# Performance work log

Hardware: AMD Instinct MI355X
Metric: run time of the kernel (lower is better)

## Reference

```python
import jax, jax.numpy as jnp
import numpy as np


def log_g(x):
    # log(relu(x) + 0.5) for x >= 0, else -softplus(-x)
    pos = jnp.log(jnp.maximum(x, 0.0) + 0.5)
    neg = -jax.nn.softplus(-x)
    return jnp.where(x >= 0, pos, neg)


def parallel_scan_log(log_coeffs, log_values):
    # h_t = a_t * h_{t-1} + b_t, computed stably in log space
    a_star = jnp.cumsum(log_coeffs, axis=1)
    log_h0_plus_b_star = jax.lax.cumlogsumexp(log_values - a_star, axis=1)
    log_h = a_star + log_h0_plus_b_star
    return jnp.exp(log_h)


def setup_inputs() -> dict:
    key = jax.random.key(0)
    k1, k2 = jax.random.split(key)
    B, S, D = 8, 4096, 1024
    x = jax.random.normal(k1, (B, S, D), dtype=jnp.float32)
    # torch nn.Linear(dim, 2*inner_dim, bias=False): weight [2*inner_dim, dim]
    W_hg = jax.random.normal(k2, (2 * D, D), dtype=jnp.float32) * (1.0 / np.sqrt(D))
    return {"x": x, "W_hg": W_hg}


def reference(x, W_hg):
    # hidden_gate projection: [B,S,D] @ [D, 2*inner] -> [B,S,2*inner]
    hg = jnp.einsum("bsd,ed->bse", x, W_hg)
    hidden, gate = jnp.split(hg, 2, axis=-1)
    log_coeffs = -jax.nn.softplus(gate)       # log(1 - z)
    log_z = -jax.nn.softplus(-gate)           # log(z)
    log_tilde_h = log_g(hidden)
    log_values = log_z + log_tilde_h
    out = parallel_scan_log(log_coeffs, log_values)
    # expansion_factor == 1.0 -> self.out is Identity; dropout_prob == 0 -> Identity
    return out
```

## Files before the change

### kernel.cpp

```cpp
#include <hip/hip_runtime.h>

#define B_   8
#define S_   4096
#define D_   1024
#define M_   (B_ * S_)
#define N_   (2 * D_)
#define K_   D_
#define CCH  128
#define LCH  32

#define BK   64
#define NT   (K_ / BK)

typedef __attribute__((ext_vector_type(8))) short bf16x8;
typedef __attribute__((ext_vector_type(4))) float f32x4;

__device__ __forceinline__ unsigned short f2bf(float f) {
  union { float f; unsigned u; } v; v.f = f;
  unsigned u = v.u;
  u = u + 0x7fffu + ((u >> 16) & 1u);
  return (unsigned short)(u >> 16);
}
__device__ __forceinline__ float bf2f(unsigned short h) {
  union { unsigned u; float f; } v; v.u = ((unsigned)h) << 16;
  return v.f;
}
__device__ __forceinline__ float sigmoidf_(float x) {
  return 1.0f / (1.0f + __expf(-x));
}

#define GLL(src, dst) __builtin_amdgcn_global_load_lds(                     \
      (const __attribute__((address_space(1))) void*)(src),                 \
      (__attribute__((address_space(3))) void*)(dst), 16, 0, 0)

__global__ __launch_bounds__(256) void k_cvt(const float* __restrict__ in,
                                             unsigned short* __restrict__ out,
                                             int n4) {
  int i = blockIdx.x * 256 + threadIdx.x;
  const int stride = gridDim.x * 256;
  for (; i < n4; i += stride) {
    float4 v = reinterpret_cast<const float4*>(in)[i];
    ushort4 o;
    o.x = f2bf(v.x); o.y = f2bf(v.y); o.z = f2bf(v.z); o.w = f2bf(v.w);
    reinterpret_cast<ushort4*>(out)[i] = o;
  }
}

__global__ __launch_bounds__(512, 2) void k_gemm(const unsigned short* __restrict__ xb,
                                                 const unsigned short* __restrict__ wb,
                                                 unsigned short* __restrict__ Gp,
                                                 unsigned short* __restrict__ Zp) {
  __shared__ unsigned short lds[65536];
  const int tid = threadIdx.x;
  int wg = blockIdx.x;
  wg = (wg & 7) * 128 + (wg >> 3);
  const int bm = wg >> 3;
  const int bn = wg & 7;
  const int lane = tid & 63;
  const int wid = tid >> 6;
  const int wr = wid >> 2;
  const int wc = wid & 3;
  const int fr = lane & 15;
  const int hi = lane >> 4;
  const int f7 = fr & 7;

  const int srow = tid >> 3;
  const int scol = ((tid & 7) ^ (srow & 7)) * 16;
  const char* aS = (const char*)xb + (size_t)(bm * 256 + srow) * 2048 + scol;
  const char* bS = (const char*)wb + (size_t)(bn * 256 + srow) * 2048 + scol;
  char* const ldsc = (char*)lds + (size_t)tid * 16;

  const int swz0 = (hi ^ f7) * 8;
  const int swz1 = ((4 + hi) ^ f7) * 8;

  f32x4 acc[8][4] = {};
  bf16x8 av[4], bv[4];

#define RD_BV(SWZ)                                                           \
  _Pragma("unroll") for (int n = 0; n < 4; ++n)                              \
    bv[n] = *(const bf16x8*)&Bb[(wc * 64 + n * 16 + fr) * 64 + (SWZ)];
#define RD_AV(MB, SWZ)                                                       \
  _Pragma("unroll") for (int m = 0; m < 4; ++m)                              \
    av[m] = *(const bf16x8*)&Ab[(wr * 128 + (MB) * 64 + m * 16 + fr) * 64 + (SWZ)];

#define STAGE4(srcbase, region)                                              \
  if (st) {                                                                  \
    GLL((srcbase) + kb,                  ldsc + bufN + (region));            \
    GLL((srcbase) + 131072 + kb,         ldsc + bufN + (region) + 8192);     \
    GLL((srcbase) + 262144 + kb,         ldsc + bufN + (region) + 16384);    \
    GLL((srcbase) + 393216 + kb,         ldsc + bufN + (region) + 24576);    \
  }

#define PHASE16(M0)                                                          \
  __builtin_amdgcn_s_barrier();                                              \
  asm volatile("s_waitcnt lgkmcnt(0)" ::: "memory");                         \
  __builtin_amdgcn_s_setprio(1);                                             \
  _Pragma("unroll") for (int m = 0; m < 4; ++m)                              \
    _Pragma("unroll") for (int n = 0; n < 4; ++n)                            \
      acc[(M0) + m][n] = __builtin_amdgcn_mfma_f32_16x16x32_bf16(            \
          av[m], bv[n], acc[(M0) + m][n], 0, 0, 0);                          \
  __builtin_amdgcn_s_setprio(0);

#pragma unroll
  for (int c = 0; c < 4; ++c) {
    GLL(aS + (size_t)c * 131072, ldsc + c * 8192);
    GLL(bS + (size_t)c * 131072, ldsc + 32768 + c * 8192);
  }
  asm volatile("s_waitcnt vmcnt(0)" ::: "memory");
  __builtin_amdgcn_s_barrier();

  for (int t = 0; t < NT; ++t) {
    const unsigned short* Ab = &lds[(t & 1) << 15];
    const unsigned short* Bb = Ab + 16384;
    const int bufN = ((t + 1) & 1) << 16;
    const size_t kb = (size_t)(t + 1) * 128;
    const bool st = (t < NT - 1);

    RD_BV(swz0);
    RD_AV(0, swz0);
    STAGE4(aS, 0);
    PHASE16(0);
    __builtin_amdgcn_s_barrier();

    RD_AV(1, swz0);
    STAGE4(bS, 32768);
    PHASE16(4);
    __builtin_amdgcn_s_barrier();

    RD_BV(swz1);
    RD_AV(0, swz1);
    PHASE16(0);
    __builtin_amdgcn_s_barrier();

    RD_AV(1, swz1);
    PHASE16(4);
    asm volatile("s_waitcnt vmcnt(0)" ::: "memory");
    __builtin_amdgcn_s_barrier();
  }

  const int row0 = bm * 256 + wr * 128 + (hi << 2);
  const int col0 = bn * 256 + wc * 64 + fr;
  if (bn < 4) {
#pragma unroll
    for (int m = 0; m < 8; ++m)
#pragma unroll
      for (int n = 0; n < 4; ++n)
#pragma unroll
        for (int i = 0; i < 4; ++i) {
          float v = acc[m][n][i];
          float g = (v >= 0.0f) ? (v + 0.5f) : sigmoidf_(v);
          Gp[(size_t)(row0 + m * 16 + i) * 1024 + (col0 + n * 16)] = f2bf(g);
        }
  } else {
#pragma unroll
    for (int m = 0; m < 8; ++m)
#pragma unroll
      for (int n = 0; n < 4; ++n)
#pragma unroll
        for (int i = 0; i < 4; ++i) {
          float v = acc[m][n][i];
          Zp[(size_t)(row0 + m * 16 + i) * 1024 + (col0 + n * 16 - 1024)] = f2bf(sigmoidf_(v));
        }
  }
}

__global__ __launch_bounds__(256) void k_scan1(const unsigned short* __restrict__ Gp,
                                               const unsigned short* __restrict__ Zp,
                                               float* __restrict__ Ap,
                                               float* __restrict__ Hp) {
  const int gid = blockIdx.x * 256 + threadIdx.x;
  const int c = blockIdx.y;
  const int b = gid >> 8;
  const int d0 = (gid & 255) << 2;
  size_t base = ((size_t)b * S_ + (size_t)c * LCH) * 1024 + d0;
  float4 aP = {1.f, 1.f, 1.f, 1.f};
  float4 h  = {0.f, 0.f, 0.f, 0.f};
#pragma unroll 8
  for (int s = 0; s < LCH; ++s) {
    ushort4 zu = *reinterpret_cast<const ushort4*>(Zp + base);
    ushort4 gu = *reinterpret_cast<const ushort4*>(Gp + base);
    float z0 = bf2f(zu.x), z1 = bf2f(zu.y), z2 = bf2f(zu.z), z3 = bf2f(zu.w);
    float a0 = 1.f - z0,   a1 = 1.f - z1,   a2 = 1.f - z2,   a3 = 1.f - z3;
    h.x = fmaf(a0, h.x, z0 * bf2f(gu.x));
    h.y = fmaf(a1, h.y, z1 * bf2f(gu.y));
    h.z = fmaf(a2, h.z, z2 * bf2f(gu.z));
    h.w = fmaf(a3, h.w, z3 * bf2f(gu.w));
    aP.x *= a0; aP.y *= a1; aP.z *= a2; aP.w *= a3;
    base += 1024;
  }
  reinterpret_cast<float4*>(Ap)[(size_t)c * 2048 + gid] = aP;
  reinterpret_cast<float4*>(Hp)[(size_t)c * 2048 + gid] = h;
}

__global__ __launch_bounds__(256) void k_scan2(const float* __restrict__ Ap,
                                               const float* __restrict__ Hp,
                                               float* __restrict__ Cin) {
  const int gid = blockIdx.x * 256 + threadIdx.x;
  float4 carry = {0.f, 0.f, 0.f, 0.f};
  for (int c = 0; c < CCH; ++c) {
    reinterpret_cast<float4*>(Cin)[(size_t)c * 2048 + gid] = carry;
    float4 a = reinterpret_cast<const float4*>(Ap)[(size_t)c * 2048 + gid];
    float4 hh = reinterpret_cast<const float4*>(Hp)[(size_t)c * 2048 + gid];
    carry.x = fmaf(a.x, carry.x, hh.x);
    carry.y = fmaf(a.y, carry.y, hh.y);
    carry.z = fmaf(a.z, carry.z, hh.z);
    carry.w = fmaf(a.w, carry.w, hh.w);
  }
}

__global__ __launch_bounds__(256) void k_scan3(const unsigned short* __restrict__ Gp,
                                               const unsigned short* __restrict__ Zp,
                                               const float* __restrict__ Cin,
                                               float* __restrict__ out) {
  const int gid = blockIdx.x * 256 + threadIdx.x;
  const int c = blockIdx.y;
  const int b = gid >> 8;
  const int d0 = (gid & 255) << 2;
  size_t base = ((size_t)b * S_ + (size_t)c * LCH) * 1024 + d0;
  float4 h = reinterpret_cast<const float4*>(Cin)[(size_t)c * 2048 + gid];
#pragma unroll 8
  for (int s = 0; s < LCH; ++s) {
    ushort4 zu = *reinterpret_cast<const ushort4*>(Zp + base);
    ushort4 gu = *reinterpret_cast<const ushort4*>(Gp + base);
    float z0 = bf2f(zu.x), z1 = bf2f(zu.y), z2 = bf2f(zu.z), z3 = bf2f(zu.w);
    h.x = fmaf(1.f - z0, h.x, z0 * bf2f(gu.x));
    h.y = fmaf(1.f - z1, h.y, z1 * bf2f(gu.y));
    h.z = fmaf(1.f - z2, h.z, z2 * bf2f(gu.z));
    h.w = fmaf(1.f - z3, h.w, z3 * bf2f(gu.w));
    *reinterpret_cast<float4*>(out + base) = h;
    base += 1024;
  }
}

extern "C" void kernel_launch(void* const* d_in, const int* in_sizes, int n_in,
                              void* d_out, int out_size, void* d_ws, size_t ws_size,
                              hipStream_t stream) {
  const float* x = (const float*)d_in[0];
  const float* W = (const float*)d_in[1];
  float* out = (float*)d_out;

  unsigned char* w = (unsigned char*)d_ws;
  unsigned short* xb = (unsigned short*)(w);
  unsigned short* wb = (unsigned short*)(w + 67108864);
  unsigned short* Gp = (unsigned short*)(w + 67108864 + 4194304);
  unsigned short* Zp = (unsigned short*)(w + 67108864 + 4194304 + 67108864);
  float* Ap  = (float*)(w);
  float* Hp  = (float*)(w + 4194304);
  float* Cin = (float*)(w + 8388608);

  k_cvt<<<4096, 256, 0, stream>>>(x, xb, (M_ * K_) / 4);
  k_cvt<<<2048, 256, 0, stream>>>(W, wb, (N_ * K_) / 4);
  k_gemm<<<(M_ / 256) * (N_ / 256), 512, 0, stream>>>(xb, wb, Gp, Zp);
  k_scan1<<<dim3(8, CCH), 256, 0, stream>>>(Gp, Zp, Ap, Hp);
  k_scan2<<<8, 256, 0, stream>>>(Ap, Hp, Cin);
  k_scan3<<<dim3(8, CCH), 256, 0, stream>>>(Gp, Zp, Cin, out);
}
```

Baseline: 273.9 us.

## Double-buffer LDS fragment registers to overlap reads with MFMA and cut barriers

Restructures the GEMM main loop so LDS-to-register fragment loads for the next MFMA phase are issued while the current phase computes. Two register sets per operand are used, and the first fragments of the next k-tile are prefetched before the last MFMA phase. This drops most of the per-phase barriers and lgkmcnt waits. The cost is higher VGPR pressure from the extra fragment registers, which may hurt occupancy or cause spills. It also relies on compiler-inserted waits for correctness.

```diff
diff --git a/kernel.cpp b/kernel.cpp
--- a/kernel.cpp
+++ b/kernel.cpp
@@ -69,36 +69,22 @@
   const char* aS = (const char*)xb + (size_t)(bm * 256 + srow) * 2048 + scol;
   const char* bS = (const char*)wb + (size_t)(bn * 256 + srow) * 2048 + scol;
   char* const ldsc = (char*)lds + (size_t)tid * 16;
-
-  const int swz0 = (hi ^ f7) * 8;
-  const int swz1 = ((4 + hi) ^ f7) * 8;
+  const char* const ldsr = (const char*)lds;
+
+  const int aoff = (wr * 128 + fr) * 128;
+  const int boff = (wc * 64 + fr) * 128;
+  const int s0 = (hi ^ f7) * 16;
+  const int s1 = ((4 + hi) ^ f7) * 16;
 
   f32x4 acc[8][4] = {};
-  bf16x8 av[4], bv[4];
-
-#define RD_BV(SWZ)                                                           \
-  _Pragma("unroll") for (int n = 0; n < 4; ++n)                              \
-    bv[n] = *(const bf16x8*)&Bb[(wc * 64 + n * 16 + fr) * 64 + (SWZ)];
-#define RD_AV(MB, SWZ)                                                       \
-  _Pragma("unroll") for (int m = 0; m < 4; ++m)                              \
-    av[m] = *(const bf16x8*)&Ab[(wr * 128 + (MB) * 64 + m * 16 + fr) * 64 + (SWZ)];
-
-#define STAGE4(srcbase, region)                                              \
-  if (st) {                                                                  \
-    GLL((srcbase) + kb,                  ldsc + bufN + (region));            \
-    GLL((srcbase) + 131072 + kb,         ldsc + bufN + (region) + 8192);     \
-    GLL((srcbase) + 262144 + kb,         ldsc + bufN + (region) + 16384);    \
-    GLL((srcbase) + 393216 + kb,         ldsc + bufN + (region) + 24576);    \
-  }
-
-#define PHASE16(M0)                                                          \
-  __builtin_amdgcn_s_barrier();                                              \
-  asm volatile("s_waitcnt lgkmcnt(0)" ::: "memory");                         \
+  bf16x8 avA[4], avB[4], bvA[4], bvB[4];
+
+#define MM16(AV, BV, O)                                                      \
   __builtin_amdgcn_s_setprio(1);                                             \
   _Pragma("unroll") for (int m = 0; m < 4; ++m)                              \
     _Pragma("unroll") for (int n = 0; n < 4; ++n)                            \
-      acc[(M0) + m][n] = __builtin_amdgcn_mfma_f32_16x16x32_bf16(            \
-          av[m], bv[n], acc[(M0) + m][n], 0, 0, 0);                          \
+      acc[(O) + m][n] = __builtin_amdgcn_mfma_f32_16x16x32_bf16(             \
+          AV[m], BV[n], acc[(O) + m][n], 0, 0, 0);                           \
   __builtin_amdgcn_s_setprio(0);
 
 #pragma unroll
@@ -106,35 +92,59 @@
     GLL(aS + (size_t)c * 131072, ldsc + c * 8192);
     GLL(bS + (size_t)c * 131072, ldsc + 32768 + c * 8192);
   }
-  asm volatile("s_waitcnt vmcnt(0)" ::: "memory");
-  __builtin_amdgcn_s_barrier();
+  asm volatile("s_waitcnt vmcnt(0)\n\ts_barrier" ::: "memory");
+#pragma unroll
+  for (int m = 0; m < 4; ++m)
+    avA[m] = *(const bf16x8*)(ldsr + aoff + m * 2048 + s0);
+#pragma unroll
+  for (int n = 0; n < 4; ++n)
+    bvA[n] = *(const bf16x8*)(ldsr + 32768 + boff + n * 2048 + s0);
 
   for (int t = 0; t < NT; ++t) {
-    const unsigned short* Ab = &lds[(t & 1) << 15];
-    const unsigned short* Bb = Ab + 16384;
-    const int bufN = ((t + 1) & 1) << 16;
+    const bool st = (t < NT - 1);
+    const char* Ab = ldsr + ((t & 1) << 16);
+    const char* Bb = Ab + 32768;
+    const char* An = ldsr + (((t + 1) & 1) << 16);
+    const char* Bn = An + 32768;
+    char* dq = ldsc + (((t + 1) & 1) << 16);
     const size_t kb = (size_t)(t + 1) * 128;
-    const bool st = (t < NT - 1);
-
-    RD_BV(swz0);
-    RD_AV(0, swz0);
-    STAGE4(aS, 0);
-    PHASE16(0);
-    __builtin_amdgcn_s_barrier();
-
-    RD_AV(1, swz0);
-    STAGE4(bS, 32768);
-    PHASE16(4);
-    __builtin_amdgcn_s_barrier();
-
-    RD_BV(swz1);
-    RD_AV(0, swz1);
-    PHASE16(0);
-    __builtin_amdgcn_s_barrier();
-
-    RD_AV(1, swz1);
-    PHASE16(4);
-    asm volatile("s_waitcnt vmcnt(0)" ::: "memory");
+
+    if (st) {
+      GLL(aS + kb, dq);                    GLL(aS + 131072 + kb, dq + 8192);
+      GLL(aS + 262144 + kb, dq + 16384);   GLL(aS + 393216 + kb, dq + 24576);
+    }
+#pragma unroll
+    for (int m = 0; m < 4; ++m)
+      avB[m] = *(const bf16x8*)(Ab + aoff + (4 + m) * 2048 + s0);
+    MM16(avA, bvA, 0);
+
+    if (st) {
+      GLL(bS + kb, dq + 32768);            GLL(bS + 131072 + kb, dq + 40960);
+      GLL(bS + 262144 + kb, dq + 49152);   GLL(bS + 393216 + kb, dq + 57344);
+    }
+#pragma unroll
+    for (int m = 0; m < 4; ++m)
+      avA[m] = *(const bf16x8*)(Ab + aoff + m * 2048 + s1);
+#pragma unroll
+    for (int n = 0; n < 4; ++n)
+      bvB[n] = *(const bf16x8*)(Bb + boff + n * 2048 + s1);
+    MM16(avB, bvA, 4);
+
+#pragma unroll
+    for (int m = 0; m < 4; ++m)
+      avB[m] = *(const bf16x8*)(Ab + aoff + (4 + m) * 2048 + s1);
+    MM16(avA, bvB, 0);
+
+    asm volatile("s_waitcnt vmcnt(0)\n\ts_barrier" ::: "memory");
+    if (st) {
+#pragma unroll
+      for (int m = 0; m < 4; ++m)
+        avA[m] = *(const bf16x8*)(An + aoff + m * 2048 + s0);
+#pragma unroll
+      for (int n = 0; n < 4; ++n)
+        bvA[n] = *(const bf16x8*)(Bn + boff + n * 2048 + s0);
+    }
+    MM16(avB, bvB, 4);
     __builtin_amdgcn_s_barrier();
   }
 
```

Measured after the change: 270.3 us. Within noise of the previous version (-1.3%).
